# Kernel optimization log

Hardware: AMD Instinct MI355X
Metric: run time of the kernel (lower is better)

## Reference

```python
import jax, jax.numpy as jnp
import numpy as np

B, S, DM = 1, 4096, 2048
H, HD = 16, 128
TS = 16          # tile_size
TOPK = 16        # anchor tiles per query
NUM_TILES = S // TS


def setup_inputs() -> dict:
    key = jax.random.key(0)
    ks = jax.random.split(key, 7)
    x = jax.random.normal(ks[0], (B, S, DM), jnp.float32)
    Wq = jax.random.normal(ks[1], (DM, H * HD), jnp.float32) * 0.02
    Wk = jax.random.normal(ks[2], (DM, H * HD), jnp.float32) * 0.02
    Wv = jax.random.normal(ks[3], (DM, H * HD), jnp.float32) * 0.02
    Wo = jax.random.normal(ks[4], (H * HD, DM), jnp.float32) * 0.02
    # RoPE angles: pos * inv_freq, shape [S, HD//2] (= freqs_cis angle)
    inv_freq = 1.0 / (10000.0 ** (np.arange(0, HD, 2, dtype=np.float32) / HD))
    freqs = jnp.asarray(np.arange(S, dtype=np.float32)[:, None] * inv_freq[None, :])
    anchor_indices = jax.random.randint(ks[5], (B, H, S, TOPK), 0, NUM_TILES).astype(jnp.int32)
    return {"x": x, "Wq": Wq, "Wk": Wk, "Wv": Wv, "Wo": Wo,
            "freqs": freqs, "anchor_indices": anchor_indices}


def _rotate_half(z):
    half = z.shape[-1] // 2
    return jnp.concatenate([-z[..., half:], z[..., :half]], axis=-1)


def reference(x, Wq, Wk, Wv, Wo, freqs, anchor_indices):
    b, s, _ = x.shape
    num_tiles = s // TS
    # QKV projections -> [B, H, S, HD]
    q = (x @ Wq).reshape(b, s, H, HD).transpose(0, 2, 1, 3)
    k = (x @ Wk).reshape(b, s, H, HD).transpose(0, 2, 1, 3)
    v = (x @ Wv).reshape(b, s, H, HD).transpose(0, 2, 1, 3)
    # RoPE (half-split / rotate_half convention), float32
    cos = jnp.cos(freqs)[None, None, :s, :]
    sin = jnp.sin(freqs)[None, None, :s, :]
    cos_full = jnp.concatenate([cos, cos], axis=-1)
    sin_full = jnp.concatenate([sin, sin], axis=-1)
    q = q * cos_full + _rotate_half(q) * sin_full
    k = k * cos_full + _rotate_half(k) * sin_full
    # Per-query tile indices: anchor tiles + local tile
    local_tiles = (jnp.arange(s) // TS).astype(jnp.int32)
    local = jnp.broadcast_to(local_tiles[None, None, :, None], (b, H, s, 1))
    tiles = jnp.concatenate([anchor_indices, local], axis=-1)  # [B,H,S,K+1]
    # Representative query per tile (last token of each query tile)
    tile_repr = jnp.arange(TS - 1, s, TS)
    tile_sel = tiles[:, :, tile_repr, :]                        # [B,H,T,K+1]
    # Expand tile indices to token indices
    offsets = jnp.arange(TS)
    token_idx = tile_sel[..., None] * TS + offsets              # [B,H,T,K+1,TS]
    sparse_len = tile_sel.shape[-1] * TS
    flat_idx = jnp.clip(token_idx.reshape(b, H, num_tiles, sparse_len), 0, s - 1)
    # Gather sparse K/V per (batch, head, query-tile)
    k_flat = k.reshape(b * H, s, HD)
    v_flat = v.reshape(b * H, s, HD)
    idx_flat = flat_idx.reshape(b * H, num_tiles, sparse_len)
    k_sparse = jax.vmap(lambda kv, idx: kv[idx])(k_flat, idx_flat)
    v_sparse = jax.vmap(lambda kv, idx: kv[idx])(v_flat, idx_flat)
    k_sparse = k_sparse.reshape(b, H, num_tiles, sparse_len, HD)
    v_sparse = v_sparse.reshape(b, H, num_tiles, sparse_len, HD)
    # Block-sparse attention per tile
    q_tiled = q.reshape(b, H, num_tiles, TS, HD)
    logits = jnp.einsum('bhtqd,bhtkd->bhtqk', q_tiled, k_sparse) / jnp.sqrt(HD)
    q_pos = jnp.arange(s).reshape(num_tiles, TS)
    future_mask = flat_idx[:, :, :, None, :] > q_pos[None, None, :, :, None]
    logits = jnp.where(future_mask, -1e10, logits)
    weights = jax.nn.softmax(logits, axis=-1)
    all_masked = jnp.all(future_mask, axis=-1, keepdims=True)
    weights = jnp.where(all_masked, 0.0, weights)
    weights = jnp.where(jnp.isnan(weights), 0.0, weights)
    out = jnp.einsum('bhtqk,bhtkd->bhtqd', weights, v_sparse)
    out = out.reshape(b, H, s, HD).transpose(0, 2, 1, 3).reshape(b, s, H * HD)
    return out @ Wo
```

## Files before the change

### kernel.cpp

```cpp
#include <hip/hip_runtime.h>

typedef unsigned short u16;
typedef unsigned int u32;
typedef __attribute__((ext_vector_type(8))) short bf16x8;
typedef __attribute__((ext_vector_type(4))) float f32x4;

__device__ __forceinline__ u16 f2bf(float f) {
  union { float f; u32 u; } v; v.f = f;
  u32 u = v.u;
  return (u16)((u + 0x7FFFu + ((u >> 16) & 1u)) >> 16);
}
__device__ __forceinline__ float bf2f(u16 s) {
  union { u32 u; float f; } v; v.u = ((u32)s) << 16;
  return v.f;
}

__device__ __forceinline__ void async16(const void* g, void* l) {
  __builtin_amdgcn_global_load_lds(
      (__attribute__((address_space(1))) void*)g,
      (__attribute__((address_space(3))) void*)l, 16, 0, 0);
}

__global__ void prep1_kernel(const float* __restrict__ x,
                             const float* __restrict__ W0, const float* __restrict__ W1,
                             const float* __restrict__ W2, const float* __restrict__ W3,
                             const float* __restrict__ freqs,
                             u16* __restrict__ xbf, u16* __restrict__ wqkvT,
                             u16* __restrict__ woT,
                             float* __restrict__ ct, float* __restrict__ st) {
  __shared__ float tile[32][33];
  const int bid = blockIdx.x;
  const int tid = threadIdx.x;
  if (bid < 16384) {
    const int z = bid >> 12;
    const float* in = z == 0 ? W0 : z == 1 ? W1 : z == 2 ? W2 : W3;
    u16* out = z == 3 ? woT : wqkvT + (size_t)z * 4194304;
    const int local = bid & 4095;
    const int c0 = (local & 63) * 32, r0 = (local >> 6) * 32;
    const int tx = tid & 31, ty = tid >> 5;
#pragma unroll
    for (int i = ty; i < 32; i += 8) tile[i][tx] = in[(size_t)(r0 + i) * 2048 + c0 + tx];
    __syncthreads();
#pragma unroll
    for (int i = ty; i < 32; i += 8)
      out[(size_t)(c0 + i) * 2048 + r0 + tx] = f2bf(tile[tx][i]);
  } else if (bid < 24576) {
    int i = (bid - 16384) * 256 + tid;
    float4 v = ((const float4*)x)[i];
    ushort4 o;
    o.x = f2bf(v.x); o.y = f2bf(v.y); o.z = f2bf(v.z); o.w = f2bf(v.w);
    ((ushort4*)xbf)[i] = o;
  } else {
    int i = (bid - 24576) * 256 + tid;
    float f = freqs[i];
    ct[i] = cosf(f); st[i] = sinf(f);
  }
}

__global__ void prep2_kernel(u16* __restrict__ q, const u16* __restrict__ k,
                             u16* __restrict__ Kp,
                             const u16* __restrict__ Vin, u16* __restrict__ VT2,
                             const float* __restrict__ ct, const float* __restrict__ st) {
  __shared__ u16 lv[64][132];
  const int bid = blockIdx.x;
  const int tid = threadIdx.x;
  if (bid < 8192) {
    int i = bid * 256 + tid;
    int dp = (i & 31) * 2;
    int hh = (i >> 5) & 15;
    int s  = i >> 9;
    float c0 = ct[s * 64 + dp], c1 = ct[s * 64 + dp + 1];
    float s0 = st[s * 64 + dp], s1 = st[s * 64 + dp + 1];
    size_t base = (size_t)s * 2048 + hh * 128 + dp;
    {
      u32 lo = *(u32*)(q + base);
      u32 hi = *(u32*)(q + base + 64);
      float a0 = bf2f((u16)lo), a1 = bf2f((u16)(lo >> 16));
      float b0 = bf2f((u16)hi), b1 = bf2f((u16)(hi >> 16));
      u32 nlo = (u32)f2bf(a0 * c0 - b0 * s0) | ((u32)f2bf(a1 * c1 - b1 * s1) << 16);
      u32 nhi = (u32)f2bf(b0 * c0 + a0 * s0) | ((u32)f2bf(b1 * c1 + a1 * s1) << 16);
      *(u32*)(q + base) = nlo;
      *(u32*)(q + base + 64) = nhi;
    }
    {
      u32 lo = *(const u32*)(k + base);
      u32 hi = *(const u32*)(k + base + 64);
      float a0 = bf2f((u16)lo), a1 = bf2f((u16)(lo >> 16));
      float b0 = bf2f((u16)hi), b1 = bf2f((u16)(hi >> 16));
      u32 nlo = (u32)f2bf(a0 * c0 - b0 * s0) | ((u32)f2bf(a1 * c1 - b1 * s1) << 16);
      u32 nhi = (u32)f2bf(b0 * c0 + a0 * s0) | ((u32)f2bf(b1 * c1 + a1 * s1) << 16);
      size_t kpb = ((size_t)hh * 4096 + s) * 128 + dp;
      *(u32*)(Kp + kpb) = nlo;
      *(u32*)(Kp + kpb + 64) = nhi;
    }
  } else {
    const int local = bid - 8192;
    const int h = local >> 6;
    const int s0 = (local & 63) * 64;
#pragma unroll
    for (int i = 0; i < 16; ++i) {
      int idx = i * 256 + tid;
      int r = idx >> 6;
      int d2 = idx & 63;
      u32 vv = ((const u32*)Vin)[(size_t)(s0 + r) * 1024 + h * 64 + d2];
      *(u32*)(&lv[r][d2 * 2]) = vv;
    }
    __syncthreads();
#pragma unroll
    for (int i = 0; i < 16; ++i) {
      int idx = i * 256 + tid;
      int k2 = idx & 7;
      int d  = (idx >> 3) & 127;
      int tl = idx >> 10;
      u32 lo = lv[tl * 16 + k2 * 2][d];
      u32 hi = lv[tl * 16 + k2 * 2 + 1][d];
      ((u32*)VT2)[(((size_t)h * 256 + (s0 >> 4) + tl) * 128 + d) * 8 + k2] = lo | (hi << 16);
    }
  }
}

template <int MODE>
__launch_bounds__(256, 2)
__global__ void gemm128_kernel(const u16* __restrict__ A, const u16* __restrict__ Bt,
                               void* __restrict__ C, u16* __restrict__ D1, u16* __restrict__ D2,
                               int M, int N, int K) {
  __shared__ __align__(16) u16 As[128 * 64];
  __shared__ __align__(16) u16 Bs[128 * 64];
  const int tid  = threadIdx.x;
  const int lane = tid & 63;
  const int wave = tid >> 6;
  const int wr = wave >> 1, wc = wave & 1;
  const int brow = blockIdx.y * 128;
  const int bcol = blockIdx.x * 128;

  int a_goff[4], b_goff[4], l_off[4];
#pragma unroll
  for (int i = 0; i < 4; ++i) {
    int p = (wave * 4 + i) * 1024 + lane * 16;
    int row = p >> 7;
    int colb = (p & 127) ^ ((row & 7) << 4);
    a_goff[i] = (brow + row) * K + (colb >> 1);
    b_goff[i] = (bcol + row) * K + (colb >> 1);
    l_off[i] = p;
  }

  f32x4 acc[4][4];
#pragma unroll
  for (int m = 0; m < 4; ++m)
#pragma unroll
    for (int n = 0; n < 4; ++n) acc[m][n] = (f32x4){0.f, 0.f, 0.f, 0.f};

  for (int k0 = 0; k0 < K; k0 += 64) {
#pragma unroll
    for (int i = 0; i < 4; ++i) {
      async16(A + a_goff[i] + k0, (char*)As + l_off[i]);
      async16(Bt + b_goff[i] + k0, (char*)Bs + l_off[i]);
    }
    __syncthreads();
#pragma unroll
    for (int kk = 0; kk < 2; ++kk) {
      bf16x8 af[4], bfr[4];
#pragma unroll
      for (int m = 0; m < 4; ++m) {
        int row = wr * 64 + m * 16 + (lane & 15);
        int byte = (row << 7) + ((kk * 64 + ((lane >> 4) << 4)) ^ ((row & 7) << 4));
        af[m] = *(const bf16x8*)((const char*)As + byte);
      }
#pragma unroll
      for (int n = 0; n < 4; ++n) {
        int row = wc * 64 + n * 16 + (lane & 15);
        int byte = (row << 7) + ((kk * 64 + ((lane >> 4) << 4)) ^ ((row & 7) << 4));
        bfr[n] = *(const bf16x8*)((const char*)Bs + byte);
      }
#pragma unroll
      for (int m = 0; m < 4; ++m)
#pragma unroll
        for (int n = 0; n < 4; ++n)
          acc[m][n] = __builtin_amdgcn_mfma_f32_16x16x32_bf16(af[m], bfr[n], acc[m][n], 0, 0, 0);
    }
    __syncthreads();
  }

  const int r0 = brow + wr * 64;
  const int c0 = bcol + wc * 64;
  if (MODE == 2) {
    const int sel = bcol >> 11;
    u16* dst = sel == 0 ? (u16*)C : sel == 1 ? D1 : D2;
    const int c0l = (bcol & 2047) + wc * 64;
#pragma unroll
    for (int m = 0; m < 4; ++m)
#pragma unroll
      for (int n = 0; n < 4; ++n)
#pragma unroll
        for (int r = 0; r < 4; ++r) {
          int rr = r0 + m * 16 + ((lane >> 4) << 2) + r;
          int cc = c0l + n * 16 + (lane & 15);
          dst[(size_t)rr * 2048 + cc] = f2bf(acc[m][n][r]);
        }
  } else {
#pragma unroll
    for (int m = 0; m < 4; ++m)
#pragma unroll
      for (int n = 0; n < 4; ++n)
#pragma unroll
        for (int r = 0; r < 4; ++r) {
          int rr = r0 + m * 16 + ((lane >> 4) << 2) + r;
          int cc = c0 + n * 16 + (lane & 15);
          if (MODE == 1) ((u16*)C)[(size_t)rr * N + cc] = f2bf(acc[m][n][r]);
          else           ((float*)C)[(size_t)rr * N + cc] = acc[m][n][r];
        }
  }
}

__launch_bounds__(256, 6)
__global__ void attn_kernel(const u16* __restrict__ Q, const u16* __restrict__ Kp,
                            const u16* __restrict__ VT2, const int* __restrict__ anchors,
                            u16* __restrict__ Out) {
  const int t = blockIdx.x;
  const int h = blockIdx.y;
  __shared__ int tiles[20];
  __shared__ __align__(16) float lg[16][292];
  const int tid  = threadIdx.x;
  const int lane = tid & 63;
  const int wave = tid >> 6;
  const int g = lane >> 4;
  const int c = lane & 15;

  if (tid < 16) tiles[tid] = anchors[(size_t)((h << 12) + (t * 16 + 15)) * 16 + tid];
  if (tid == 16) tiles[16] = t;
  if (tid >= 17 && tid < 20) tiles[tid] = 0;
  __syncthreads();

  {
    const u16* qbase = Q + (size_t)(t * 16 + c) * 2048 + h * 128 + g * 8;
    bf16x8 qf[4];
#pragma unroll
    for (int ks = 0; ks < 4; ++ks) qf[ks] = *(const bf16x8*)(qbase + ks * 32);

    int tok_[5];
    const u16* kb_[5];
#pragma unroll
    for (int i = 0; i < 5; ++i) {
      int j = wave + 4 * i;
      tok_[i] = tiles[j] * 16 + c;
      kb_[i] = Kp + ((size_t)h * 4096 + tok_[i]) * 128 + g * 8;
    }
    bf16x8 kfp[2][4];
#pragma unroll
    for (int ks = 0; ks < 4; ++ks) kfp[0][ks] = *(const bf16x8*)(kb_[0] + ks * 32);
#pragma unroll
    for (int i = 0; i < 5; ++i) {
      if (i < 4) {
#pragma unroll
        for (int ks = 0; ks < 4; ++ks)
          kfp[(i + 1) & 1][ks] = *(const bf16x8*)(kb_[i + 1] + ks * 32);
      }
      f32x4 a = (f32x4){0.f, 0.f, 0.f, 0.f};
#pragma unroll
      for (int ks = 0; ks < 4; ++ks)
        a = __builtin_amdgcn_mfma_f32_16x16x32_bf16(qf[ks], kfp[i & 1][ks], a, 0, 0, 0);
      int j = wave + 4 * i;
      if (j < 17) {
#pragma unroll
        for (int r = 0; r < 4; ++r) {
          int qrow = g * 4 + r;
          float vv = a[r] * 0.088388347648318447f;
          if (tok_[i] > t * 16 + qrow) vv = -1e10f;
          lg[qrow][j * 16 + c] = vv;
        }
      }
    }
  }
  __syncthreads();

  {
    const int r = tid >> 4, cc = tid & 15;
    float vals[17];
    float mx = -3.0e38f;
#pragma unroll
    for (int i = 0; i < 17; ++i) { vals[i] = lg[r][i * 16 + cc]; mx = fmaxf(mx, vals[i]); }
#pragma unroll
    for (int d = 1; d < 16; d <<= 1) mx = fmaxf(mx, __shfl_xor(mx, d, 64));
    float sum = 0.f;
#pragma unroll
    for (int i = 0; i < 17; ++i) { vals[i] = __expf(vals[i] - mx); sum += vals[i]; }
#pragma unroll
    for (int d = 1; d < 16; d <<= 1) sum += __shfl_xor(sum, d, 64);
    float inv = sum > 0.f ? 1.0f / sum : 0.f;
    u16* wrow = (u16*)&lg[r][0];
#pragma unroll
    for (int i = 0; i < 17; ++i) wrow[i * 16 + cc] = f2bf(vals[i] * inv);
    wrow[272 + cc] = 0;
  }
  __syncthreads();

  {
    f32x4 o0 = (f32x4){0.f, 0.f, 0.f, 0.f}, o1 = o0;
    const int d0 = wave * 32;
    const size_t hb = (size_t)h * 256;
    const int keyin = (g & 1) * 8;
    const u16* wrow = (const u16*)&lg[c][0];
    const u16* vb_[9];
#pragma unroll
    for (int ks = 0; ks < 9; ++ks) vb_[ks] = VT2 + (hb + tiles[2 * ks + (g >> 1)]) * 2048;
    bf16x8 pb0[2], pb1[2];
    pb0[0] = *(const bf16x8*)(vb_[0] + (d0 + c) * 16 + keyin);
    pb1[0] = *(const bf16x8*)(vb_[0] + (d0 + 16 + c) * 16 + keyin);
#pragma unroll
    for (int ks = 0; ks < 9; ++ks) {
      if (ks < 8) {
        pb0[(ks + 1) & 1] = *(const bf16x8*)(vb_[ks + 1] + (d0 + c) * 16 + keyin);
        pb1[(ks + 1) & 1] = *(const bf16x8*)(vb_[ks + 1] + (d0 + 16 + c) * 16 + keyin);
      }
      bf16x8 af = *(const bf16x8*)(wrow + ks * 32 + g * 8);
      o0 = __builtin_amdgcn_mfma_f32_16x16x32_bf16(af, pb0[ks & 1], o0, 0, 0, 0);
      o1 = __builtin_amdgcn_mfma_f32_16x16x32_bf16(af, pb1[ks & 1], o1, 0, 0, 0);
    }
#pragma unroll
    for (int r = 0; r < 4; ++r) {
      int qrow = g * 4 + r;
      size_t base = (size_t)(t * 16 + qrow) * 2048 + h * 128;
      Out[base + d0 + c]      = f2bf(o0[r]);
      Out[base + d0 + 16 + c] = f2bf(o1[r]);
    }
  }
}

extern "C" void kernel_launch(void* const* d_in, const int* in_sizes, int n_in,
                              void* d_out, int out_size, void* d_ws, size_t ws_size,
                              hipStream_t stream) {
  (void)in_sizes; (void)n_in; (void)out_size; (void)ws_size;
  const float* x      = (const float*)d_in[0];
  const float* Wq     = (const float*)d_in[1];
  const float* Wk     = (const float*)d_in[2];
  const float* Wv     = (const float*)d_in[3];
  const float* Wo     = (const float*)d_in[4];
  const float* freqs  = (const float*)d_in[5];
  const int* anchors  = (const int*)d_in[6];
  float* out = (float*)d_out;

  char* ws = (char*)d_ws;
  const size_t MB = 1024 * 1024;
  u16* xbf   = (u16*)(ws + 0);
  u16* wqkvT = (u16*)(ws + 16 * MB);
  u16* woT   = (u16*)(ws + 40 * MB);
  u16* qbf   = (u16*)(ws + 48 * MB);
  u16* kbf   = (u16*)(ws + 64 * MB);
  u16* vbf   = (u16*)(ws + 80 * MB);
  u16* attnb = (u16*)(ws + 0);
  u16* Kp    = (u16*)(ws + 16 * MB);
  u16* VT2   = (u16*)(ws + 64 * MB);
  float* ct  = (float*)(ws + 96 * MB);
  float* st  = (float*)(ws + 97 * MB);

  prep1_kernel<<<25600, 256, 0, stream>>>(x, Wq, Wk, Wv, Wo, freqs,
                                          xbf, wqkvT, woT, ct, st);
  gemm128_kernel<2><<<dim3(48, 32), 256, 0, stream>>>(xbf, wqkvT, qbf, kbf, vbf,
                                                      4096, 6144, 2048);
  prep2_kernel<<<9216, 256, 0, stream>>>(qbf, kbf, Kp, vbf, VT2, ct, st);
  attn_kernel<<<dim3(256, 16), 256, 0, stream>>>(qbf, Kp, VT2, anchors, attnb);
  gemm128_kernel<0><<<dim3(16, 32), 256, 0, stream>>>(attnb, woT, out, nullptr, nullptr,
                                                      4096, 2048, 2048);
}
```

Measured before the change: 241.0 us.

## Use 8-wave triple-buffered GEMM and fuse Q RoPE into attention

Replaces the 128x128 four-wave GEMM with a 128x256 tile, eight-wave kernel. It uses a three-stage LDS ring with async global-to-LDS loads issued two tiles ahead, split MFMA phases, explicit barriers and s_setprio, so loads overlap compute. Separately, the Q RoPE rotation moves out of prep2 into the attention kernel's Q-fragment load, which drops a read-modify-write pass over Q. The cost is higher LDS use (one block per CU) and hand-tuned waitcnt counts that must match the number of issued loads.

After: 256.4 us. +6.4%, slower.

```diff
diff --git a/kernel.cpp b/kernel.cpp
--- a/kernel.cpp
+++ b/kernel.cpp
@@ -57,8 +57,7 @@
   }
 }
 
-__global__ void prep2_kernel(u16* __restrict__ q, const u16* __restrict__ k,
-                             u16* __restrict__ Kp,
+__global__ void prep2_kernel(const u16* __restrict__ k, u16* __restrict__ Kp,
                              const u16* __restrict__ Vin, u16* __restrict__ VT2,
                              const float* __restrict__ ct, const float* __restrict__ st) {
   __shared__ u16 lv[64][132];
@@ -72,27 +71,15 @@
     float c0 = ct[s * 64 + dp], c1 = ct[s * 64 + dp + 1];
     float s0 = st[s * 64 + dp], s1 = st[s * 64 + dp + 1];
     size_t base = (size_t)s * 2048 + hh * 128 + dp;
-    {
-      u32 lo = *(u32*)(q + base);
-      u32 hi = *(u32*)(q + base + 64);
-      float a0 = bf2f((u16)lo), a1 = bf2f((u16)(lo >> 16));
-      float b0 = bf2f((u16)hi), b1 = bf2f((u16)(hi >> 16));
-      u32 nlo = (u32)f2bf(a0 * c0 - b0 * s0) | ((u32)f2bf(a1 * c1 - b1 * s1) << 16);
-      u32 nhi = (u32)f2bf(b0 * c0 + a0 * s0) | ((u32)f2bf(b1 * c1 + a1 * s1) << 16);
-      *(u32*)(q + base) = nlo;
-      *(u32*)(q + base + 64) = nhi;
-    }
-    {
-      u32 lo = *(const u32*)(k + base);
-      u32 hi = *(const u32*)(k + base + 64);
-      float a0 = bf2f((u16)lo), a1 = bf2f((u16)(lo >> 16));
-      float b0 = bf2f((u16)hi), b1 = bf2f((u16)(hi >> 16));
-      u32 nlo = (u32)f2bf(a0 * c0 - b0 * s0) | ((u32)f2bf(a1 * c1 - b1 * s1) << 16);
-      u32 nhi = (u32)f2bf(b0 * c0 + a0 * s0) | ((u32)f2bf(b1 * c1 + a1 * s1) << 16);
-      size_t kpb = ((size_t)hh * 4096 + s) * 128 + dp;
-      *(u32*)(Kp + kpb) = nlo;
-      *(u32*)(Kp + kpb + 64) = nhi;
-    }
+    u32 lo = *(const u32*)(k + base);
+    u32 hi = *(const u32*)(k + base + 64);
+    float a0 = bf2f((u16)lo), a1 = bf2f((u16)(lo >> 16));
+    float b0 = bf2f((u16)hi), b1 = bf2f((u16)(hi >> 16));
+    u32 nlo = (u32)f2bf(a0 * c0 - b0 * s0) | ((u32)f2bf(a1 * c1 - b1 * s1) << 16);
+    u32 nhi = (u32)f2bf(b0 * c0 + a0 * s0) | ((u32)f2bf(b1 * c1 + a1 * s1) << 16);
+    size_t kpb = ((size_t)hh * 4096 + s) * 128 + dp;
+    *(u32*)(Kp + kpb) = nlo;
+    *(u32*)(Kp + kpb + 64) = nhi;
   } else {
     const int local = bid - 8192;
     const int h = local >> 6;
@@ -120,28 +107,36 @@
 }
 
 template <int MODE>
-__launch_bounds__(256, 2)
-__global__ void gemm128_kernel(const u16* __restrict__ A, const u16* __restrict__ Bt,
-                               void* __restrict__ C, u16* __restrict__ D1, u16* __restrict__ D2,
-                               int M, int N, int K) {
-  __shared__ __align__(16) u16 As[128 * 64];
-  __shared__ __align__(16) u16 Bs[128 * 64];
-  const int tid  = threadIdx.x;
+__launch_bounds__(512, 1)
+__global__ void gemm8p_kernel(const u16* __restrict__ A, const u16* __restrict__ Bt,
+                              void* __restrict__ C, u16* __restrict__ D1, u16* __restrict__ D2,
+                              int M, int N, int K) {
+  __shared__ __align__(16) u16 As[3][128 * 64];
+  __shared__ __align__(16) u16 Bs[3][256 * 64];
+  const int tid = threadIdx.x;
   const int lane = tid & 63;
   const int wave = tid >> 6;
-  const int wr = wave >> 1, wc = wave & 1;
+  const int wm = wave >> 2, wn = wave & 3;
+  const int c = lane & 15, g = lane >> 4;
   const int brow = blockIdx.y * 128;
-  const int bcol = blockIdx.x * 128;
-
-  int a_goff[4], b_goff[4], l_off[4];
-#pragma unroll
-  for (int i = 0; i < 4; ++i) {
-    int p = (wave * 4 + i) * 1024 + lane * 16;
+  const int bcol = blockIdx.x * 256;
+
+  int a_g[2], a_l[2], b_g[4], b_l[4];
+#pragma unroll
+  for (int i = 0; i < 2; ++i) {
+    int p = i * 8192 + tid * 16;
     int row = p >> 7;
     int colb = (p & 127) ^ ((row & 7) << 4);
-    a_goff[i] = (brow + row) * K + (colb >> 1);
-    b_goff[i] = (bcol + row) * K + (colb >> 1);
-    l_off[i] = p;
+    a_g[i] = (brow + row) * K + (colb >> 1);
+    a_l[i] = p;
+  }
+#pragma unroll
+  for (int i = 0; i < 4; ++i) {
+    int p = i * 8192 + tid * 16;
+    int row = p >> 7;
+    int colb = (p & 127) ^ ((row & 7) << 4);
+    b_g[i] = (bcol + row) * K + (colb >> 1);
+    b_l[i] = p;
   }
 
   f32x4 acc[4][4];
@@ -150,64 +145,130 @@
 #pragma unroll
     for (int n = 0; n < 4; ++n) acc[m][n] = (f32x4){0.f, 0.f, 0.f, 0.f};
 
-  for (int k0 = 0; k0 < K; k0 += 64) {
-#pragma unroll
-    for (int i = 0; i < 4; ++i) {
-      async16(A + a_goff[i] + k0, (char*)As + l_off[i]);
-      async16(Bt + b_goff[i] + k0, (char*)Bs + l_off[i]);
-    }
-    __syncthreads();
-#pragma unroll
-    for (int kk = 0; kk < 2; ++kk) {
-      bf16x8 af[4], bfr[4];
-#pragma unroll
-      for (int m = 0; m < 4; ++m) {
-        int row = wr * 64 + m * 16 + (lane & 15);
-        int byte = (row << 7) + ((kk * 64 + ((lane >> 4) << 4)) ^ ((row & 7) << 4));
-        af[m] = *(const bf16x8*)((const char*)As + byte);
-      }
-#pragma unroll
-      for (int n = 0; n < 4; ++n) {
-        int row = wc * 64 + n * 16 + (lane & 15);
-        int byte = (row << 7) + ((kk * 64 + ((lane >> 4) << 4)) ^ ((row & 7) << 4));
-        bfr[n] = *(const bf16x8*)((const char*)Bs + byte);
-      }
+  const int nt = K >> 6;
+#pragma unroll
+  for (int i = 0; i < 2; ++i) async16(A + a_g[i], (char*)As[0] + a_l[i]);
+#pragma unroll
+  for (int i = 0; i < 4; ++i) async16(Bt + b_g[i], (char*)Bs[0] + b_l[i]);
+#pragma unroll
+  for (int i = 0; i < 2; ++i) async16(A + a_g[i] + 64, (char*)As[1] + a_l[i]);
+#pragma unroll
+  for (int i = 0; i < 4; ++i) async16(Bt + b_g[i] + 64, (char*)Bs[1] + b_l[i]);
+  asm volatile("s_waitcnt vmcnt(6)" ::: "memory");
+  __builtin_amdgcn_sched_barrier(0);
+  __builtin_amdgcn_s_barrier();
+
+  int cur = 0;
+  for (int t = 0; t < nt; ++t) {
+    const int b = cur;
+    int sb = cur + 2; if (sb >= 3) sb -= 3;
+    const bool nb2 = (t + 2) < nt;
+    const int k2 = (t + 2) << 6;
+    const char* Ab = (const char*)As[b];
+    const char* Bb = (const char*)Bs[b];
+
+    bf16x8 af[2][4], b01[2][2], b23[2][2];
+#pragma unroll
+    for (int m = 0; m < 4; ++m) {
+      const int row = wm * 64 + m * 16 + c;
+      const int rb = row << 7;
+      const int sw = (row & 7) << 4;
+#pragma unroll
+      for (int ks = 0; ks < 2; ++ks)
+        af[ks][m] = *(const bf16x8*)(Ab + rb + ((ks * 64 + (g << 4)) ^ sw));
+    }
+#pragma unroll
+    for (int n = 0; n < 2; ++n) {
+      const int row = wn * 64 + n * 16 + c;
+      const int rb = row << 7;
+      const int sw = (row & 7) << 4;
+#pragma unroll
+      for (int ks = 0; ks < 2; ++ks)
+        b01[ks][n] = *(const bf16x8*)(Bb + rb + ((ks * 64 + (g << 4)) ^ sw));
+    }
+    if (nb2) {
+      async16(A + a_g[0] + k2, (char*)As[sb] + a_l[0]);
+      async16(A + a_g[1] + k2, (char*)As[sb] + a_l[1]);
+      async16(Bt + b_g[0] + k2, (char*)Bs[sb] + b_l[0]);
+    }
+    __builtin_amdgcn_sched_barrier(0);
+    __builtin_amdgcn_s_barrier();
+    asm volatile("s_waitcnt lgkmcnt(0)" ::: "memory");
+    __builtin_amdgcn_sched_barrier(0);
+    __builtin_amdgcn_s_setprio(1);
+#pragma unroll
+    for (int ks = 0; ks < 2; ++ks)
 #pragma unroll
       for (int m = 0; m < 4; ++m)
 #pragma unroll
-        for (int n = 0; n < 4; ++n)
-          acc[m][n] = __builtin_amdgcn_mfma_f32_16x16x32_bf16(af[m], bfr[n], acc[m][n], 0, 0, 0);
-    }
-    __syncthreads();
-  }
-
-  const int r0 = brow + wr * 64;
-  const int c0 = bcol + wc * 64;
+        for (int n = 0; n < 2; ++n)
+          acc[m][n] = __builtin_amdgcn_mfma_f32_16x16x32_bf16(af[ks][m], b01[ks][n], acc[m][n], 0, 0, 0);
+    __builtin_amdgcn_s_setprio(0);
+    __builtin_amdgcn_sched_barrier(0);
+    __builtin_amdgcn_s_barrier();
+
+#pragma unroll
+    for (int n = 0; n < 2; ++n) {
+      const int row = wn * 64 + (n + 2) * 16 + c;
+      const int rb = row << 7;
+      const int sw = (row & 7) << 4;
+#pragma unroll
+      for (int ks = 0; ks < 2; ++ks)
+        b23[ks][n] = *(const bf16x8*)(Bb + rb + ((ks * 64 + (g << 4)) ^ sw));
+    }
+    if (nb2) {
+      async16(Bt + b_g[1] + k2, (char*)Bs[sb] + b_l[1]);
+      async16(Bt + b_g[2] + k2, (char*)Bs[sb] + b_l[2]);
+      async16(Bt + b_g[3] + k2, (char*)Bs[sb] + b_l[3]);
+      asm volatile("s_waitcnt vmcnt(6)" ::: "memory");
+    } else if (t + 1 < nt) {
+      asm volatile("s_waitcnt vmcnt(0)" ::: "memory");
+    }
+    __builtin_amdgcn_sched_barrier(0);
+    __builtin_amdgcn_s_barrier();
+    asm volatile("s_waitcnt lgkmcnt(0)" ::: "memory");
+    __builtin_amdgcn_sched_barrier(0);
+    __builtin_amdgcn_s_setprio(1);
+#pragma unroll
+    for (int ks = 0; ks < 2; ++ks)
+#pragma unroll
+      for (int m = 0; m < 4; ++m)
+#pragma unroll
+        for (int n = 0; n < 2; ++n)
+          acc[m][n + 2] = __builtin_amdgcn_mfma_f32_16x16x32_bf16(af[ks][m], b23[ks][n], acc[m][n + 2], 0, 0, 0);
+    __builtin_amdgcn_s_setprio(0);
+    __builtin_amdgcn_sched_barrier(0);
+    __builtin_amdgcn_s_barrier();
+
+    cur += 1; if (cur == 3) cur = 0;
+  }
+
+  const int r0 = brow + wm * 64;
   if (MODE == 2) {
     const int sel = bcol >> 11;
     u16* dst = sel == 0 ? (u16*)C : sel == 1 ? D1 : D2;
-    const int c0l = (bcol & 2047) + wc * 64;
+    const int c0l = (bcol & 2047) + wn * 64;
 #pragma unroll
     for (int m = 0; m < 4; ++m)
 #pragma unroll
       for (int n = 0; n < 4; ++n)
 #pragma unroll
         for (int r = 0; r < 4; ++r) {
-          int rr = r0 + m * 16 + ((lane >> 4) << 2) + r;
-          int cc = c0l + n * 16 + (lane & 15);
+          int rr = r0 + m * 16 + g * 4 + r;
+          int cc = c0l + n * 16 + c;
           dst[(size_t)rr * 2048 + cc] = f2bf(acc[m][n][r]);
         }
   } else {
+    const int c0 = bcol + wn * 64;
 #pragma unroll
     for (int m = 0; m < 4; ++m)
 #pragma unroll
       for (int n = 0; n < 4; ++n)
 #pragma unroll
         for (int r = 0; r < 4; ++r) {
-          int rr = r0 + m * 16 + ((lane >> 4) << 2) + r;
-          int cc = c0 + n * 16 + (lane & 15);
-          if (MODE == 1) ((u16*)C)[(size_t)rr * N + cc] = f2bf(acc[m][n][r]);
-          else           ((float*)C)[(size_t)rr * N + cc] = acc[m][n][r];
+          int rr = r0 + m * 16 + g * 4 + r;
+          int cc = c0 + n * 16 + c;
+          ((float*)C)[(size_t)rr * N + cc] = acc[m][n][r];
         }
   }
 }
@@ -215,7 +276,8 @@
 __launch_bounds__(256, 6)
 __global__ void attn_kernel(const u16* __restrict__ Q, const u16* __restrict__ Kp,
                             const u16* __restrict__ VT2, const int* __restrict__ anchors,
-                            u16* __restrict__ Out) {
+                            u16* __restrict__ Out,
+                            const float* __restrict__ ct, const float* __restrict__ st) {
   const int t = blockIdx.x;
   const int h = blockIdx.y;
   __shared__ int tiles[20];
@@ -232,10 +294,32 @@
   __syncthreads();
 
   {
-    const u16* qbase = Q + (size_t)(t * 16 + c) * 2048 + h * 128 + g * 8;
+    const int s = t * 16 + c;
+    const u16* qbase = Q + (size_t)s * 2048 + h * 128 + g * 8;
+    bf16x8 qr[4];
+#pragma unroll
+    for (int ks = 0; ks < 4; ++ks) qr[ks] = *(const bf16x8*)(qbase + ks * 32);
+    float c0[8], s0[8], c1[8], s1[8];
+    const float* ctb = ct + s * 64;
+    const float* stb = st + s * 64;
+    *(float4*)&c0[0] = *(const float4*)(ctb + g * 8);
+    *(float4*)&c0[4] = *(const float4*)(ctb + g * 8 + 4);
+    *(float4*)&c1[0] = *(const float4*)(ctb + 32 + g * 8);
+    *(float4*)&c1[4] = *(const float4*)(ctb + 32 + g * 8 + 4);
+    *(float4*)&s0[0] = *(const float4*)(stb + g * 8);
+    *(float4*)&s0[4] = *(const float4*)(stb + g * 8 + 4);
+    *(float4*)&s1[0] = *(const float4*)(stb + 32 + g * 8);
+    *(float4*)&s1[4] = *(const float4*)(stb + 32 + g * 8 + 4);
     bf16x8 qf[4];
 #pragma unroll
-    for (int ks = 0; ks < 4; ++ks) qf[ks] = *(const bf16x8*)(qbase + ks * 32);
+    for (int j = 0; j < 8; ++j) {
+      float f0 = bf2f((u16)qr[0][j]), f1 = bf2f((u16)qr[1][j]);
+      float f2 = bf2f((u16)qr[2][j]), f3 = bf2f((u16)qr[3][j]);
+      qf[0][j] = (short)f2bf(f0 * c0[j] - f2 * s0[j]);
+      qf[1][j] = (short)f2bf(f1 * c1[j] - f3 * s1[j]);
+      qf[2][j] = (short)f2bf(f2 * c0[j] + f0 * s0[j]);
+      qf[3][j] = (short)f2bf(f3 * c1[j] + f1 * s1[j]);
+    }
 
     int tok_[5];
     const u16* kb_[5];
@@ -355,10 +439,10 @@
 
   prep1_kernel<<<25600, 256, 0, stream>>>(x, Wq, Wk, Wv, Wo, freqs,
                                           xbf, wqkvT, woT, ct, st);
-  gemm128_kernel<2><<<dim3(48, 32), 256, 0, stream>>>(xbf, wqkvT, qbf, kbf, vbf,
-                                                      4096, 6144, 2048);
-  prep2_kernel<<<9216, 256, 0, stream>>>(qbf, kbf, Kp, vbf, VT2, ct, st);
-  attn_kernel<<<dim3(256, 16), 256, 0, stream>>>(qbf, Kp, VT2, anchors, attnb);
-  gemm128_kernel<0><<<dim3(16, 32), 256, 0, stream>>>(attnb, woT, out, nullptr, nullptr,
-                                                      4096, 2048, 2048);
-}
+  gemm8p_kernel<2><<<dim3(24, 32), 512, 0, stream>>>(xbf, wqkvT, qbf, kbf, vbf,
+                                                     4096, 6144, 2048);
+  prep2_kernel<<<9216, 256, 0, stream>>>(kbf, Kp, vbf, VT2, ct, st);
+  attn_kernel<<<dim3(256, 16), 256, 0, stream>>>(qbf, Kp, VT2, anchors, attnb, ct, st);
+  gemm8p_kernel<0><<<dim3(8, 32), 512, 0, stream>>>(attnb, woT, out, nullptr, nullptr,
+                                                    4096, 2048, 2048);
+}
```
